# Kernel optimization log

Measured on AMD Instinct MI355X. Metric: run time of the kernel, lower is better.

Reference implementation:

```python
import jax, jax.numpy as jnp
import numpy as np

N = 25600            # 64 graphs x 400 ROIs
F_IN = 400
H = 128
E = 512000           # 8000 edges per graph
B = 64
G = 8
OUT = 2
NPG = 400            # nodes per graph
EPG = E // B         # edges per graph
BN_EPS = 1e-5


def _xavier(k, shape):
    lim = float(np.sqrt(6.0 / (shape[0] + shape[1])))
    return jax.random.uniform(k, shape, jnp.float32, -lim, lim)


def setup_inputs() -> dict:
    key = jax.random.key(0)
    ks = jax.random.split(key, 16)
    inp = {}
    inp["x"] = jax.random.normal(ks[0], (N, F_IN), jnp.float32)
    # within-graph random edges: local index + graph offset
    src_l = jax.random.randint(ks[1], (E,), 0, NPG, jnp.int32)
    dst_l = jax.random.randint(ks[2], (E,), 0, NPG, jnp.int32)
    off = (jnp.arange(E, dtype=jnp.int32) // EPG) * NPG
    inp["edge_index"] = jnp.stack([src_l + off, dst_l + off])
    inp["batch"] = (jnp.arange(N, dtype=jnp.int32) // NPG)
    inp["group_ids"] = jax.random.randint(ks[3], (N,), 0, G, jnp.int32)
    inp["ge"] = _xavier(ks[4], (G, 2))
    inp["he"] = _xavier(ks[5], (2, 2))
    dims = [(F_IN + 4, H), (H, H), (H, H)]
    for i, (di, do) in enumerate(dims):
        k1, k2 = jax.random.split(ks[6 + i])
        inp[f"w{i}a"] = _xavier(k1, (di, do))
        inp[f"b{i}a"] = jnp.zeros((do,), jnp.float32)
        inp[f"g{i}"] = jnp.ones((do,), jnp.float32)
        inp[f"be{i}"] = jnp.zeros((do,), jnp.float32)
        inp[f"w{i}b"] = _xavier(k2, (do, do))
        inp[f"b{i}b"] = jnp.zeros((do,), jnp.float32)
    inp["wfa"] = _xavier(ks[10], (H, H))
    inp["bfa"] = jnp.zeros((H,), jnp.float32)
    inp["wfb"] = _xavier(ks[11], (H, OUT))
    inp["bfb"] = jnp.zeros((OUT,), jnp.float32)
    return inp


def _bn(h, gamma, beta):
    # BatchNorm1d in training mode: stats over node dimension
    mu = jnp.mean(h, axis=0, keepdims=True)
    var = jnp.var(h, axis=0, keepdims=True)
    return gamma * (h - mu) * jax.lax.rsqrt(var + BN_EPS) + beta


def reference(x, edge_index, batch, group_ids, ge, he,
              w0a, b0a, g0, be0, w0b, b0b,
              w1a, b1a, g1, be1, w1b, b1b,
              w2a, b2a, g2, be2, w2b, b2b,
              wfa, bfa, wfb, bfb):
    n = x.shape[0]
    hemi = jnp.arange(n) % 2                      # [1::2] = 1
    h = jnp.concatenate([x, ge[group_ids], he[hemi]], axis=-1)  # [N, F_IN+4]
    src, dst = edge_index[0], edge_index[1]
    layers = [(w0a, b0a, g0, be0, w0b, b0b),
              (w1a, b1a, g1, be1, w1b, b1b),
              (w2a, b2a, g2, be2, w2b, b2b)]
    for wa, ba, g, be, wb, bb in layers:
        # GINConv (eps=0): x_i + sum_{(j,i)} x_j, then 2-layer MLP w/ batchnorm
        agg = jax.ops.segment_sum(h[src], dst, num_segments=N)
        z = h + agg
        z = jax.nn.relu(_bn(z @ wa + ba, g, be))  # dropout = identity (eval)
        h = jax.nn.relu(z @ wb + bb)              # outer ReLU from forward()
    pooled = jax.ops.segment_sum(h, batch, num_segments=B)  # global_add_pool
    return jax.nn.relu(pooled @ wfa + bfa) @ wfb + bfb
```

## Files before the change

### kernel.cpp

```cpp
#include <hip/hip_runtime.h>

#define N_NODES 25600
#define F_IN 400
#define NE 512000
#define NB 64
#define NPG 400
#define EPG 8000
#define BN_EPS 1e-5f
#define NBLK 256

typedef __attribute__((ext_vector_type(8))) short short8;
typedef __attribute__((ext_vector_type(4))) float floatx4;
typedef unsigned short us;
typedef unsigned long long u64;

__device__ __forceinline__ unsigned short f2bf(float f) {
    unsigned int u = __float_as_uint(f);
    u += 0x7FFF + ((u >> 16) & 1);
    return (unsigned short)(u >> 16);
}
__device__ __forceinline__ float bf2f(unsigned short s) {
    return __uint_as_float((unsigned int)s << 16);
}
__device__ __forceinline__ short u8bf(unsigned v) {
    return (short)(__float_as_uint((float)v) >> 16);
}
__device__ __forceinline__ void ast64(void* p, u64 v) {
    __hip_atomic_store((u64*)p, v, __ATOMIC_RELAXED, __HIP_MEMORY_SCOPE_AGENT);
}
__device__ __forceinline__ u64 pk4(unsigned short a, unsigned short b, unsigned short c, unsigned short d) {
    return (u64)a | ((u64)b << 16) | ((u64)c << 32) | ((u64)d << 48);
}

__device__ __forceinline__ void gsync_tree(unsigned* bar, int bid, int phase) {
    __syncthreads();
    if (threadIdx.x == 0) {
        unsigned* leaf = bar + 32 + (bid >> 4) * 32;
        unsigned v = __hip_atomic_fetch_add(leaf, 1u, __ATOMIC_RELAXED, __HIP_MEMORY_SCOPE_AGENT);
        if (v == (unsigned)(phase * 16 - 1))
            __hip_atomic_fetch_add(bar, 1u, __ATOMIC_RELAXED, __HIP_MEMORY_SCOPE_AGENT);
        while (__hip_atomic_load(bar, __ATOMIC_RELAXED, __HIP_MEMORY_SCOPE_AGENT) < (unsigned)(phase * 16))
            __builtin_amdgcn_s_sleep(8);
        asm volatile("" ::: "memory");
    }
    __syncthreads();
}

__device__ __forceinline__ void gbar4(unsigned* gc, int stage) {
    __syncthreads();
    if (threadIdx.x == 0) {
        __hip_atomic_fetch_add(gc, 1u, __ATOMIC_RELAXED, __HIP_MEMORY_SCOPE_AGENT);
        while (__hip_atomic_load(gc, __ATOMIC_RELAXED, __HIP_MEMORY_SCOPE_AGENT) < (unsigned)(stage * 4))
            __builtin_amdgcn_s_sleep(8);
        asm volatile("" ::: "memory");
    }
    __syncthreads();
}



__device__ __forceinline__ void ph_prep(unsigned char* sm, int g, int q, int bid, int tid,
        const int* __restrict__ src, const int* __restrict__ dst, us* __restrict__ SbBF,
        const float* __restrict__ wa0, const float* __restrict__ wa1, const float* __restrict__ wa2,
        const float* __restrict__ wb0, const float* __restrict__ wb1, const float* __restrict__ wb2,
        us* __restrict__ wt0, us* __restrict__ wtb0, us* __restrict__ wta1,
        us* __restrict__ wtb1, us* __restrict__ wta2, us* __restrict__ wtb2) {
    int r0 = q * 112;
    int* cnt = (int*)sm;
    for (int i = tid; i < 11200; i += 1024) cnt[i] = 0;
    __syncthreads();
    int ebase = g * EPG, nbase = g * NPG;
    for (int e = tid; e < EPG; e += 1024) {
        int d = dst[ebase + e] - nbase;
        int dr = d - r0;
        if ((unsigned)dr < 112u) {
            int s = src[ebase + e] - nbase;
            int idx = dr * NPG + s;
            atomicAdd(&cnt[idx >> 2], (int)(1u << ((idx & 3) * 8)));
        }
    }
    __syncthreads();
    const unsigned char* cb = (const unsigned char*)cnt;
    for (int i = tid; i < 112 * 112; i += 1024) {
        int rr = i / 112, c4 = (i % 112) * 4;
        int R = r0 + rr;
        ushort4 o;
#pragma unroll
        for (int j = 0; j < 4; ++j) {
            int c = c4 + j;
            unsigned v = (R < NPG && c < NPG) ? (unsigned)cb[rr * NPG + c] + (c == R ? 1u : 0u) : 0u;
            ((unsigned short*)&o)[j] = (unsigned short)u8bf(v);
        }
        *(ushort4*)&SbBF[((size_t)g * 448 + R) * 448 + c4] = o;
    }
    if (tid < 136) {
        int idx = bid * 136 + tid;
        if (idx < 14336) {
            int n = idx / 112, k0 = (idx % 112) * 4;
            unsigned short o[4];
#pragma unroll
            for (int j = 0; j < 4; ++j) {
                int k = k0 + j;
                o[j] = (k < 400) ? f2bf(wa0[(size_t)k * 128 + n]) : (unsigned short)0;
            }
            ast64(&wt0[(size_t)n * 448 + k0], pk4(o[0], o[1], o[2], o[3]));
        } else {
            int r2 = idx - 14336;
            int m = r2 >> 12, q2 = r2 & 4095;
            int n = q2 >> 5, k0 = (q2 & 31) * 4;
            const float* smat = (m == 0) ? wb0 : (m == 1) ? wa1 : (m == 2) ? wb1 : (m == 3) ? wa2 : wb2;
            us* dmat = (m == 0) ? wtb0 : (m == 1) ? wta1 : (m == 2) ? wtb1 : (m == 3) ? wta2 : wtb2;
            unsigned short o[4];
#pragma unroll
            for (int j = 0; j < 4; ++j) o[j] = f2bf(smat[(size_t)(k0 + j) * 128 + n]);
            ast64(&dmat[(size_t)n * 128 + k0], pk4(o[0], o[1], o[2], o[3]));
        }
    }
}


__device__ __forceinline__ void ph_embed(unsigned char* sm, int g, int q, int tid,
        const float* __restrict__ x, const us* __restrict__ wt0, const float* __restrict__ wa0,
        const int* __restrict__ gid, const float* __restrict__ ge, const float* __restrict__ he,
        us* __restrict__ tT0) {
    us (*Bf)[456] = (us(*)[456])sm;
    us (*As)[72] = (us(*)[72])(sm + 116736);
    float (*Wex)[128] = (float(*)[128])(sm + 135168);
    int nb = g * NPG + q * 100;
    int wave = tid >> 6, lane = tid & 63;
    int wrow = wave >> 2, wc4 = wave & 3;
    int fm = lane & 15, quad = lane >> 4;

    {
        short8 tp[7];
#pragma unroll
        for (int j = 0; j < 7; ++j) {
            int i = tid + j * 1024;
            int col = i / 56, kq = (i - col * 56) * 8;
            tp[j] = *(const short8*)(wt0 + (size_t)col * 448 + kq);
        }
#pragma unroll
        for (int j = 0; j < 7; ++j) {
            int i = tid + j * 1024;
            int col = i / 56, kq = (i - col * 56) * 8;
            *(short8*)&Bf[col][kq] = tp[j];
        }
    }
    for (int i = tid; i < 512; i += 1024)
        Wex[i >> 7][i & 127] = wa0[(size_t)(400 + (i >> 7)) * 128 + (i & 127)];

    floatx4 acc[2][2];
#pragma unroll
    for (int rt = 0; rt < 2; ++rt)
#pragma unroll
        for (int ct = 0; ct < 2; ++ct) acc[rt][ct] = (floatx4){0.f, 0.f, 0.f, 0.f};

    const int rA = tid >> 3, kcA = (tid & 7) * 8;
    float v[8];
    auto loadK = [&](int ks) {
        int kg = ks * 64 + kcA;
        if (rA < 100) {
            const float* ar = x + (size_t)(nb + rA) * F_IN;
            if (kg + 7 < 400) {
                float4 a = *(const float4*)(ar + kg);
                float4 b = *(const float4*)(ar + kg + 4);
                v[0] = a.x; v[1] = a.y; v[2] = a.z; v[3] = a.w;
                v[4] = b.x; v[5] = b.y; v[6] = b.z; v[7] = b.w;
            } else {
#pragma unroll
                for (int j = 0; j < 8; ++j) v[j] = (kg + j < 400) ? ar[kg + j] : 0.f;
            }
        } else {
#pragma unroll
            for (int j = 0; j < 8; ++j) v[j] = 0.f;
        }
    };

    loadK(0);
    for (int ks = 0; ks < 7; ++ks) {
        {
            short8 s;
#pragma unroll
            for (int j = 0; j < 8; ++j) s[j] = (short)f2bf(v[j]);
            *(short8*)&As[rA][kcA] = s;
        }
        __syncthreads();
        if (ks + 1 < 7) loadK(ks + 1);
#pragma unroll
        for (int k0l = 0; k0l < 64; k0l += 32) {
            short8 af[2], bf[2];
#pragma unroll
            for (int rt = 0; rt < 2; ++rt)
                af[rt] = *(const short8*)&As[wrow * 32 + rt * 16 + fm][k0l + quad * 8];
#pragma unroll
            for (int ct = 0; ct < 2; ++ct)
                bf[ct] = *(const short8*)&Bf[wc4 * 32 + ct * 16 + fm][ks * 64 + k0l + quad * 8];
#pragma unroll
            for (int rt = 0; rt < 2; ++rt)
#pragma unroll
                for (int ct = 0; ct < 2; ++ct)
                    acc[rt][ct] = __builtin_amdgcn_mfma_f32_16x16x32_bf16(
                        af[rt], bf[ct], acc[rt][ct], 0, 0, 0);
        }
        __syncthreads();
    }

#pragma unroll
    for (int rt = 0; rt < 2; ++rt)
#pragma unroll
        for (int ct = 0; ct < 2; ++ct) {
            int col = wc4 * 32 + ct * 16 + fm;
            int rl0 = wrow * 32 + rt * 16 + quad * 4;
            if (rl0 < 100) {
                unsigned short o[4];
#pragma unroll
                for (int r = 0; r < 4; ++r) {
                    int row = nb + rl0 + r;
                    int gv = gid[row];
                    float vv = acc[rt][ct][r]
                             + ge[gv * 2] * Wex[0][col] + ge[gv * 2 + 1] * Wex[1][col]
                             + he[(row & 1) * 2] * Wex[2][col] + he[(row & 1) * 2 + 1] * Wex[3][col];
                    o[r] = f2bf(vv);
                }
                ast64(&tT0[(size_t)col * N_NODES + nb + rl0], pk4(o[0], o[1], o[2], o[3]));
            }
        }
}


__device__ __forceinline__ void ph_agg(unsigned char* sm, int g, int q, int tid,
        const us* __restrict__ SbBF, const us* __restrict__ tTr, const float* __restrict__ ba,
        float* __restrict__ psum, float* __restrict__ psq, int bucket) {
    us (*Bf)[456] = (us(*)[456])sm;
    us (*zl)[136] = (us(*)[136])sm;
    float (*rs)[4][2][16] = (float(*)[4][2][16])(sm + 116736);
    float (*rq)[4][2][16] = (float(*)[4][2][16])(sm + 118784);
    int wave = tid >> 6, lane = tid & 63;
    int wrow = wave >> 2, wc4 = wave & 3;
    int fm = lane & 15, quad = lane >> 4;
    int node0 = g * NPG;

    {
        short8 tp[7];
        const short8 z8 = {0, 0, 0, 0, 0, 0, 0, 0};
#pragma unroll
        for (int j = 0; j < 7; ++j) {
            int i = tid + j * 1024;
            int col = i / 56, kq = (i - col * 56) * 8;
            tp[j] = (kq < 400) ? *(const short8*)(tTr + (size_t)col * N_NODES + node0 + kq) : z8;
        }
#pragma unroll
        for (int j = 0; j < 7; ++j) {
            int i = tid + j * 1024;
            int col = i / 56, kq = (i - col * 56) * 8;
            *(short8*)&Bf[col][kq] = tp[j];
        }
    }
    __syncthreads();

    floatx4 acc[2][2];
#pragma unroll
    for (int rt = 0; rt < 2; ++rt)
#pragma unroll
        for (int ct = 0; ct < 2; ++ct) acc[rt][ct] = (floatx4){0.f, 0.f, 0.f, 0.f};

    const us* abase = SbBF + ((size_t)g * 448 + q * 112) * 448;
#pragma unroll
    for (int ks = 0; ks < 7; ++ks) {
#pragma unroll
        for (int k0l = 0; k0l < 64; k0l += 32) {
            short8 af[2], bf[2];
#pragma unroll
            for (int rt = 0; rt < 2; ++rt)
                af[rt] = *(const short8*)(abase + (size_t)(wrow * 32 + rt * 16 + fm) * 448
                                          + ks * 64 + k0l + quad * 8);
#pragma unroll
            for (int ct = 0; ct < 2; ++ct)
                bf[ct] = *(const short8*)&Bf[wc4 * 32 + ct * 16 + fm][ks * 64 + k0l + quad * 8];
#pragma unroll
            for (int rt = 0; rt < 2; ++rt)
#pragma unroll
                for (int ct = 0; ct < 2; ++ct)
                    acc[rt][ct] = __builtin_amdgcn_mfma_f32_16x16x32_bf16(
                        af[rt], bf[ct], acc[rt][ct], 0, 0, 0);
        }
    }
    __syncthreads();

    int nrows = (q < 3) ? 112 : 64;
    float sc[2] = {0.f, 0.f}, sq2[2] = {0.f, 0.f};
#pragma unroll
    for (int rt = 0; rt < 2; ++rt)
#pragma unroll
        for (int ct = 0; ct < 2; ++ct) {
            int col = wc4 * 32 + ct * 16 + fm;
            int rl0 = wrow * 32 + rt * 16 + quad * 4;
            if (rl0 < nrows) {
                float bv = ba[col];
#pragma unroll
                for (int r = 0; r < 4; ++r) {
                    float vv = acc[rt][ct][r] + bv;
                    zl[rl0 + r][col] = f2bf(vv);
                    sc[ct] += vv;
                    sq2[ct] += vv * vv;
                }
            }
        }
#pragma unroll
    for (int ct = 0; ct < 2; ++ct) {
        sc[ct] += __shfl_xor(sc[ct], 16);
        sc[ct] += __shfl_xor(sc[ct], 32);
        sq2[ct] += __shfl_xor(sq2[ct], 16);
        sq2[ct] += __shfl_xor(sq2[ct], 32);
    }
    if (lane < 16) {
#pragma unroll
        for (int ct = 0; ct < 2; ++ct) { rs[wrow][wc4][ct][lane] = sc[ct]; rq[wrow][wc4][ct][lane] = sq2[ct]; }
    }
    __syncthreads();
    if (tid < 128) {
        int wc = tid >> 5, ct = (tid >> 4) & 1, f = tid & 15;
        float S = 0.f, Q = 0.f;
#pragma unroll
        for (int wr = 0; wr < 4; ++wr) { S += rs[wr][wc][ct][f]; Q += rq[wr][wc][ct][f]; }
        atomicAdd(&psum[bucket * 128 + tid], S);
        atomicAdd(&psq[bucket * 128 + tid], Q);
    }
}


template <int FINAL>
__device__ __forceinline__ void ph_post(unsigned char* sm, int g, int q, int tid,
        const float* __restrict__ psum, const float* __restrict__ psq,
        const float* __restrict__ gamma, const float* __restrict__ beta,
        const us* __restrict__ wtbP, const float* __restrict__ bb,
        const us* __restrict__ wanP, us* __restrict__ tTw, float& p0, float& p1) {
    us (*zl)[136] = (us(*)[136])sm;
    float* coefs = (float*)(sm + 34816);
    us (*Bw)[136] = (us(*)[136])(sm + 35840);
    int wave = tid >> 6, lane = tid & 63;
    int wrow = wave >> 2, wc4 = wave & 3;
    int fm = lane & 15, quad = lane >> 4;
    int nrows = (q < 3) ? 112 : 64;
    int nb = g * NPG + q * 112;

    short8 w1[2], w2[2];
#pragma unroll
    for (int j = 0; j < 2; ++j) {
        int i = tid + j * 1024;
        int col = i >> 4, kq = (i & 15) * 8;
        w1[j] = *(const short8*)(wtbP + (size_t)col * 128 + kq);
        if (!FINAL) w2[j] = *(const short8*)(wanP + (size_t)col * 128 + kq);
    }

    if (tid < 128) {
        float S = 0.f, Q = 0.f;
#pragma unroll
        for (int b = 0; b < 16; ++b) {
            S += __hip_atomic_load(&psum[b * 128 + tid], __ATOMIC_RELAXED, __HIP_MEMORY_SCOPE_AGENT);
            Q += __hip_atomic_load(&psq[b * 128 + tid], __ATOMIC_RELAXED, __HIP_MEMORY_SCOPE_AGENT);
        }
        float invn = 1.0f / (float)N_NODES;
        float mu = S * invn;
        float var = Q * invn - mu * mu;
        float a = gamma[tid] * rsqrtf(var + BN_EPS);
        coefs[tid] = a;
        coefs[128 + tid] = beta[tid] - a * mu;
    }
#pragma unroll
    for (int j = 0; j < 2; ++j) {
        int i = tid + j * 1024;
        int col = i >> 4, kq = (i & 15) * 8;
        *(short8*)&Bw[col][kq] = w1[j];
    }
    __syncthreads();
    for (int i = tid; i < 16384; i += 1024) {
        int rl = i >> 7, col = i & 127;
        float vv = bf2f(zl[rl][col]);
        zl[rl][col] = f2bf(fmaxf(coefs[col] * vv + coefs[128 + col], 0.f));
    }
    __syncthreads();

    floatx4 acc[2][2];
#pragma unroll
    for (int rt = 0; rt < 2; ++rt)
#pragma unroll
        for (int ct = 0; ct < 2; ++ct) acc[rt][ct] = (floatx4){0.f, 0.f, 0.f, 0.f};

#pragma unroll
    for (int ks = 0; ks < 2; ++ks)
#pragma unroll
        for (int k0l = 0; k0l < 64; k0l += 32) {
            short8 af[2], bf[2];
#pragma unroll
            for (int rt = 0; rt < 2; ++rt)
                af[rt] = *(const short8*)&zl[wrow * 32 + rt * 16 + fm][ks * 64 + k0l + quad * 8];
#pragma unroll
            for (int ct = 0; ct < 2; ++ct)
                bf[ct] = *(const short8*)&Bw[wc4 * 32 + ct * 16 + fm][ks * 64 + k0l + quad * 8];
#pragma unroll
            for (int rt = 0; rt < 2; ++rt)
#pragma unroll
                for (int ct = 0; ct < 2; ++ct)
                    acc[rt][ct] = __builtin_amdgcn_mfma_f32_16x16x32_bf16(
                        af[rt], bf[ct], acc[rt][ct], 0, 0, 0);
        }

    if (FINAL) {
#pragma unroll
        for (int rt = 0; rt < 2; ++rt)
#pragma unroll
            for (int ct = 0; ct < 2; ++ct) {
                int col = wc4 * 32 + ct * 16 + fm;
                int rl0 = wrow * 32 + rt * 16 + quad * 4;
                if (rl0 < nrows) {
                    float bv = bb[col];
                    float s = 0.f;
#pragma unroll
                    for (int r = 0; r < 4; ++r) s += fmaxf(acc[rt][ct][r] + bv, 0.f);
                    if (ct == 0) p0 += s; else p1 += s;
                }
            }
        return;
    }

    __syncthreads();
#pragma unroll
    for (int rt = 0; rt < 2; ++rt)
#pragma unroll
        for (int ct = 0; ct < 2; ++ct) {
            int col = wc4 * 32 + ct * 16 + fm;
            float bv = bb[col];
            int rl0 = wrow * 32 + rt * 16 + quad * 4;
#pragma unroll
            for (int r = 0; r < 4; ++r)
                zl[rl0 + r][col] = f2bf(fmaxf(acc[rt][ct][r] + bv, 0.f));
        }
#pragma unroll
    for (int j = 0; j < 2; ++j) {
        int i = tid + j * 1024;
        int col = i >> 4, kq = (i & 15) * 8;
        *(short8*)&Bw[col][kq] = w2[j];
    }
    __syncthreads();

#pragma unroll
    for (int rt = 0; rt < 2; ++rt)
#pragma unroll
        for (int ct = 0; ct < 2; ++ct) acc[rt][ct] = (floatx4){0.f, 0.f, 0.f, 0.f};

#pragma unroll
    for (int ks = 0; ks < 2; ++ks)
#pragma unroll
        for (int k0l = 0; k0l < 64; k0l += 32) {
            short8 af[2], bf[2];
#pragma unroll
            for (int rt = 0; rt < 2; ++rt)
                af[rt] = *(const short8*)&zl[wrow * 32 + rt * 16 + fm][ks * 64 + k0l + quad * 8];
#pragma unroll
            for (int ct = 0; ct < 2; ++ct)
                bf[ct] = *(const short8*)&Bw[wc4 * 32 + ct * 16 + fm][ks * 64 + k0l + quad * 8];
#pragma unroll
            for (int rt = 0; rt < 2; ++rt)
#pragma unroll
                for (int ct = 0; ct < 2; ++ct)
                    acc[rt][ct] = __builtin_amdgcn_mfma_f32_16x16x32_bf16(
                        af[rt], bf[ct], acc[rt][ct], 0, 0, 0);
        }

#pragma unroll
    for (int rt = 0; rt < 2; ++rt)
#pragma unroll
        for (int ct = 0; ct < 2; ++ct) {
            int col = wc4 * 32 + ct * 16 + fm;
            int rl0 = wrow * 32 + rt * 16 + quad * 4;
            if (rl0 < nrows) {
                unsigned short o[4];
#pragma unroll
                for (int r = 0; r < 4; ++r) o[r] = f2bf(acc[rt][ct][r]);
                ast64(&tTw[(size_t)col * N_NODES + nb + rl0], pk4(o[0], o[1], o[2], o[3]));
            }
        }
}


__global__ __launch_bounds__(1024, 4) void persist_all(
        const float* __restrict__ x, const int* __restrict__ esrc, const int* __restrict__ edst,
        const int* __restrict__ gid, const float* __restrict__ ge, const float* __restrict__ he,
        const float* __restrict__ wa0, const float* __restrict__ ba0, const float* __restrict__ gg0,
        const float* __restrict__ be0, const float* __restrict__ wb0, const float* __restrict__ bbias0,
        const float* __restrict__ wa1, const float* __restrict__ ba1, const float* __restrict__ gg1,
        const float* __restrict__ be1, const float* __restrict__ wb1, const float* __restrict__ bbias1,
        const float* __restrict__ wa2, const float* __restrict__ ba2, const float* __restrict__ gg2,
        const float* __restrict__ be2, const float* __restrict__ wb2, const float* __restrict__ bbias2,
        const float* __restrict__ wfa, const float* __restrict__ bfa,
        const float* __restrict__ wfb, const float* __restrict__ bfb,
        us* __restrict__ tT0, us* __restrict__ tT1, us* __restrict__ tT2,
        us* __restrict__ SbBF, float* __restrict__ pstat, unsigned* __restrict__ bar,
        us* __restrict__ wt0, us* __restrict__ wtb0, us* __restrict__ wta1,
        us* __restrict__ wtb1, us* __restrict__ wta2, us* __restrict__ wtb2,
        float* __restrict__ out) {
    __shared__ __align__(16) unsigned char sm[137216];
    int bid = blockIdx.x, tid = threadIdx.x;
    int g = (bid & 7) * 8 + ((bid >> 3) & 7);
    int q = bid >> 6;
    unsigned* gc = bar + 544 + g * 32;
    float* pooled = pstat + 12288;
    float p0 = 0.f, p1 = 0.f;

    ph_prep(sm, g, q, bid, tid, esrc, edst, SbBF, wa0, wa1, wa2, wb0, wb1, wb2,
            wt0, wtb0, wta1, wtb1, wta2, wtb2);
    gsync_tree(bar, bid, 1);

    ph_embed(sm, g, q, tid, x, wt0, wa0, gid, ge, he, tT0);
    gbar4(gc, 1);

    ph_agg(sm, g, q, tid, SbBF, tT0, ba0, pstat + 0, pstat + 2048, bid & 15);
    gsync_tree(bar, bid, 2);
    ph_post<0>(sm, g, q, tid, pstat + 0, pstat + 2048, gg0, be0, wtb0, bbias0, wta1, tT1, p0, p1);
    gbar4(gc, 2);

    ph_agg(sm, g, q, tid, SbBF, tT1, ba1, pstat + 4096, pstat + 6144, bid & 15);
    gsync_tree(bar, bid, 3);
    ph_post<0>(sm, g, q, tid, pstat + 4096, pstat + 6144, gg1, be1, wtb1, bbias1, wta2, tT2, p0, p1);
    gbar4(gc, 3);

    ph_agg(sm, g, q, tid, SbBF, tT2, ba2, pstat + 8192, pstat + 10240, bid & 15);
    gsync_tree(bar, bid, 4);
    ph_post<1>(sm, g, q, tid, pstat + 8192, pstat + 10240, gg2, be2, wtb2, bbias2, nullptr, nullptr, p0, p1);

    {
        int wave = tid >> 6, lane = tid & 63;
        int wrow = wave >> 2, wc4 = wave & 3;
        float (*red)[4][2][16] = (float(*)[4][2][16])sm;
        p0 += __shfl_xor(p0, 16); p0 += __shfl_xor(p0, 32);
        p1 += __shfl_xor(p1, 16); p1 += __shfl_xor(p1, 32);
        __syncthreads();
        if (lane < 16) { red[wrow][wc4][0][lane] = p0; red[wrow][wc4][1][lane] = p1; }
        __syncthreads();
        if (tid < 128) {
            int wc = tid >> 5, ct = (tid >> 4) & 1, f = tid & 15;
            float s = 0.f;
#pragma unroll
            for (int wr = 0; wr < 4; ++wr) s += red[wr][wc][ct][f];
            atomicAdd(&pooled[g * 128 + tid], s);
        }
    }
    gbar4(gc, 4);

    if (q == 0) {
        float* pl = (float*)sm;
        float* o0 = pl + 128;
        float* o1 = pl + 256;
        __syncthreads();
        if (tid < 128) {
            unsigned uv = __hip_atomic_load((const unsigned*)&pooled[g * 128 + tid],
                                            __ATOMIC_RELAXED, __HIP_MEMORY_SCOPE_AGENT);
            pl[tid] = __uint_as_float(uv);
        }
        __syncthreads();
        if (tid < 128) {
            float a = bfa[tid];
            for (int k = 0; k < 128; ++k) a += pl[k] * wfa[k * 128 + tid];
            float p2 = fmaxf(a, 0.f);
            o0[tid] = p2 * wfb[tid * 2 + 0];
            o1[tid] = p2 * wfb[tid * 2 + 1];
        }
        __syncthreads();
        if (tid == 0) {
            float a0 = bfb[0], a1 = bfb[1];
#pragma unroll
            for (int k = 0; k < 128; ++k) { a0 += o0[k]; a1 += o1[k]; }
            out[g * 2 + 0] = a0;
            out[g * 2 + 1] = a1;
        }
    }
}


extern "C" void kernel_launch(void* const* d_in, const int* in_sizes, int n_in,
                              void* d_out, int out_size, void* d_ws, size_t ws_size,
                              hipStream_t stream) {
    const float* x   = (const float*)d_in[0];
    const int* ei    = (const int*)d_in[1];
    const int* gid   = (const int*)d_in[3];
    const float* ge  = (const float*)d_in[4];
    const float* he  = (const float*)d_in[5];
    float* out = (float*)d_out;

    char* ws = (char*)d_ws;
    size_t o = 0;
    auto alloc = [&](size_t bytes) { char* p = ws + o; o += (bytes + 255) & ~(size_t)255; return p; };
    size_t tbytes = (size_t)128 * N_NODES * 2;
    us* tT0 = (us*)alloc(tbytes);
    us* tT1 = (us*)alloc(tbytes);
    us* tT2 = (us*)alloc(tbytes);
    us* SbBF = (us*)alloc((size_t)NB * 448 * 448 * 2);
    float* pstat = (float*)alloc(20480 * 4);
    unsigned* bar = (unsigned*)alloc(12288);
    us* wt0  = (us*)alloc(128 * 448 * 2);
    us* wtb0 = (us*)alloc(128 * 128 * 2);
    us* wta1 = (us*)alloc(128 * 128 * 2);
    us* wtb1 = (us*)alloc(128 * 128 * 2);
    us* wta2 = (us*)alloc(128 * 128 * 2);
    us* wtb2 = (us*)alloc(128 * 128 * 2);
    (void)ws_size; (void)in_sizes; (void)n_in; (void)out_size;

    hipMemsetAsync(pstat, 0, 81920 + 12288, stream);

    persist_all<<<NBLK, 1024, 0, stream>>>(
        x, ei, ei + NE, gid, ge, he,
        (const float*)d_in[6],  (const float*)d_in[7],  (const float*)d_in[8],
        (const float*)d_in[9],  (const float*)d_in[10], (const float*)d_in[11],
        (const float*)d_in[12], (const float*)d_in[13], (const float*)d_in[14],
        (const float*)d_in[15], (const float*)d_in[16], (const float*)d_in[17],
        (const float*)d_in[18], (const float*)d_in[19], (const float*)d_in[20],
        (const float*)d_in[21], (const float*)d_in[22], (const float*)d_in[23],
        (const float*)d_in[24], (const float*)d_in[25],
        (const float*)d_in[26], (const float*)d_in[27],
        tT0, tT1, tT2, SbBF, pstat, bar,
        wt0, wtb0, wta1, wtb1, wta2, wtb2,
        out);
}
```

Before: 248.1 us.

## Pack adjacency to 4-bit counts and keep block's slice resident in LDS

The per-graph dense adjacency (edge counts plus identity) is now stored as 4-bit nibbles instead of bf16. Each block loads its 112-row slice once into shared memory after the embed phase and reuses it for all three aggregation layers. This replaces repeated global reads of a large bf16 matrix with per-element nibble-to-bf16 unpacking in the MFMA loop and a larger LDS footprint. It risks wrong results if any multi-edge count plus self-loop reaches 16, and the larger LDS use may lower occupancy.

```diff
diff --git a/kernel.cpp b/kernel.cpp
--- a/kernel.cpp
+++ b/kernel.cpp
@@ -9,6 +9,9 @@
 #define BN_EPS 1e-5f
 #define NBLK 256
 
+#define A4OFF 129024
+#define SM_SIZE 158720
+
 typedef __attribute__((ext_vector_type(8))) short short8;
 typedef __attribute__((ext_vector_type(4))) float floatx4;
 typedef unsigned short us;
@@ -60,7 +63,7 @@
 
 
 __device__ __forceinline__ void ph_prep(unsigned char* sm, int g, int q, int bid, int tid,
-        const int* __restrict__ src, const int* __restrict__ dst, us* __restrict__ SbBF,
+        const int* __restrict__ src, const int* __restrict__ dst, unsigned char* __restrict__ Sb4,
         const float* __restrict__ wa0, const float* __restrict__ wa1, const float* __restrict__ wa2,
         const float* __restrict__ wb0, const float* __restrict__ wb1, const float* __restrict__ wb2,
         us* __restrict__ wt0, us* __restrict__ wtb0, us* __restrict__ wta1,
@@ -81,17 +84,17 @@
     }
     __syncthreads();
     const unsigned char* cb = (const unsigned char*)cnt;
-    for (int i = tid; i < 112 * 112; i += 1024) {
-        int rr = i / 112, c4 = (i % 112) * 4;
+    for (int i = tid; i < 112 * 56; i += 1024) {
+        int rr = i / 56, c8 = (i % 56) * 8;
         int R = r0 + rr;
-        ushort4 o;
-#pragma unroll
-        for (int j = 0; j < 4; ++j) {
-            int c = c4 + j;
+        unsigned pk = 0;
+#pragma unroll
+        for (int j = 0; j < 8; ++j) {
+            int c = c8 + j;
             unsigned v = (R < NPG && c < NPG) ? (unsigned)cb[rr * NPG + c] + (c == R ? 1u : 0u) : 0u;
-            ((unsigned short*)&o)[j] = (unsigned short)u8bf(v);
-        }
-        *(ushort4*)&SbBF[((size_t)g * 448 + R) * 448 + c4] = o;
+            pk |= (v & 15u) << (4 * j);
+        }
+        *(unsigned*)&Sb4[(size_t)g * 100352 + (size_t)R * 224 + (c8 >> 1)] = pk;
     }
     if (tid < 136) {
         int idx = bid * 136 + tid;
@@ -229,12 +232,13 @@
 
 
 __device__ __forceinline__ void ph_agg(unsigned char* sm, int g, int q, int tid,
-        const us* __restrict__ SbBF, const us* __restrict__ tTr, const float* __restrict__ ba,
+        const us* __restrict__ tTr, const float* __restrict__ ba,
         float* __restrict__ psum, float* __restrict__ psq, int bucket) {
     us (*Bf)[456] = (us(*)[456])sm;
     us (*zl)[136] = (us(*)[136])sm;
     float (*rs)[4][2][16] = (float(*)[4][2][16])(sm + 116736);
     float (*rq)[4][2][16] = (float(*)[4][2][16])(sm + 118784);
+    const unsigned char* A4 = sm + A4OFF;
     int wave = tid >> 6, lane = tid & 63;
     int wrow = wave >> 2, wc4 = wave & 3;
     int fm = lane & 15, quad = lane >> 4;
@@ -264,16 +268,20 @@
 #pragma unroll
         for (int ct = 0; ct < 2; ++ct) acc[rt][ct] = (floatx4){0.f, 0.f, 0.f, 0.f};
 
-    const us* abase = SbBF + ((size_t)g * 448 + q * 112) * 448;
 #pragma unroll
     for (int ks = 0; ks < 7; ++ks) {
 #pragma unroll
         for (int k0l = 0; k0l < 64; k0l += 32) {
             short8 af[2], bf[2];
 #pragma unroll
-            for (int rt = 0; rt < 2; ++rt)
-                af[rt] = *(const short8*)(abase + (size_t)(wrow * 32 + rt * 16 + fm) * 448
-                                          + ks * 64 + k0l + quad * 8);
+            for (int rt = 0; rt < 2; ++rt) {
+                int row = wrow * 32 + rt * 16 + fm;
+                unsigned aP = *(const unsigned*)(A4 + row * 232 + ks * 32 + (k0l >> 1) + quad * 4);
+                short8 s;
+#pragma unroll
+                for (int j = 0; j < 8; ++j) s[j] = u8bf((aP >> (4 * j)) & 15u);
+                af[rt] = s;
+            }
 #pragma unroll
             for (int ct = 0; ct < 2; ++ct)
                 bf[ct] = *(const short8*)&Bf[wc4 * 32 + ct * 16 + fm][ks * 64 + k0l + quad * 8];
@@ -496,11 +504,11 @@
         const float* __restrict__ wfa, const float* __restrict__ bfa,
         const float* __restrict__ wfb, const float* __restrict__ bfb,
         us* __restrict__ tT0, us* __restrict__ tT1, us* __restrict__ tT2,
-        us* __restrict__ SbBF, float* __restrict__ pstat, unsigned* __restrict__ bar,
+        unsigned char* __restrict__ Sb4, float* __restrict__ pstat, unsigned* __restrict__ bar,
         us* __restrict__ wt0, us* __restrict__ wtb0, us* __restrict__ wta1,
         us* __restrict__ wtb1, us* __restrict__ wta2, us* __restrict__ wtb2,
         float* __restrict__ out) {
-    __shared__ __align__(16) unsigned char sm[137216];
+    __shared__ __align__(16) unsigned char sm[SM_SIZE];
     int bid = blockIdx.x, tid = threadIdx.x;
     int g = (bid & 7) * 8 + ((bid >> 3) & 7);
     int q = bid >> 6;
@@ -508,24 +516,44 @@
     float* pooled = pstat + 12288;
     float p0 = 0.f, p1 = 0.f;
 
-    ph_prep(sm, g, q, bid, tid, esrc, edst, SbBF, wa0, wa1, wa2, wb0, wb1, wb2,
+    ph_prep(sm, g, q, bid, tid, esrc, edst, Sb4, wa0, wa1, wa2, wb0, wb1, wb2,
             wt0, wtb0, wta1, wtb1, wta2, wtb2);
     gsync_tree(bar, bid, 1);
 
     ph_embed(sm, g, q, tid, x, wt0, wa0, gid, ge, he, tT0);
+
+    u64 aP4[4];
+    {
+        const u64* gs = (const u64*)(Sb4 + (size_t)g * 100352 + (size_t)q * 25088);
+#pragma unroll
+        for (int j = 0; j < 4; ++j) {
+            int i = tid + j * 1024;
+            aP4[j] = (i < 3136) ? gs[i] : 0ull;
+        }
+    }
     gbar4(gc, 1);
-
-    ph_agg(sm, g, q, tid, SbBF, tT0, ba0, pstat + 0, pstat + 2048, bid & 15);
+    {
+#pragma unroll
+        for (int j = 0; j < 4; ++j) {
+            int i = tid + j * 1024;
+            if (i < 3584) {
+                int rr = i / 28, c = i - rr * 28;
+                *(u64*)(sm + A4OFF + rr * 232 + c * 8) = aP4[j];
+            }
+        }
+    }
+
+    ph_agg(sm, g, q, tid, tT0, ba0, pstat + 0, pstat + 2048, bid & 15);
     gsync_tree(bar, bid, 2);
     ph_post<0>(sm, g, q, tid, pstat + 0, pstat + 2048, gg0, be0, wtb0, bbias0, wta1, tT1, p0, p1);
     gbar4(gc, 2);
 
-    ph_agg(sm, g, q, tid, SbBF, tT1, ba1, pstat + 4096, pstat + 6144, bid & 15);
+    ph_agg(sm, g, q, tid, tT1, ba1, pstat + 4096, pstat + 6144, bid & 15);
     gsync_tree(bar, bid, 3);
     ph_post<0>(sm, g, q, tid, pstat + 4096, pstat + 6144, gg1, be1, wtb1, bbias1, wta2, tT2, p0, p1);
     gbar4(gc, 3);
 
-    ph_agg(sm, g, q, tid, SbBF, tT2, ba2, pstat + 8192, pstat + 10240, bid & 15);
+    ph_agg(sm, g, q, tid, tT2, ba2, pstat + 8192, pstat + 10240, bid & 15);
     gsync_tree(bar, bid, 4);
     ph_post<1>(sm, g, q, tid, pstat + 8192, pstat + 10240, gg2, be2, wtb2, bbias2, nullptr, nullptr, p0, p1);
 
@@ -595,7 +623,7 @@
     us* tT0 = (us*)alloc(tbytes);
     us* tT1 = (us*)alloc(tbytes);
     us* tT2 = (us*)alloc(tbytes);
-    us* SbBF = (us*)alloc((size_t)NB * 448 * 448 * 2);
+    unsigned char* Sb4 = (unsigned char*)alloc((size_t)NB * 100352);
     float* pstat = (float*)alloc(20480 * 4);
     unsigned* bar = (unsigned*)alloc(12288);
     us* wt0  = (us*)alloc(128 * 448 * 2);
@@ -618,7 +646,7 @@
         (const float*)d_in[21], (const float*)d_in[22], (const float*)d_in[23],
         (const float*)d_in[24], (const float*)d_in[25],
         (const float*)d_in[26], (const float*)d_in[27],
-        tT0, tT1, tT2, SbBF, pstat, bar,
+        tT0, tT1, tT2, Sb4, pstat, bar,
         wt0, wtb0, wta1, wtb1, wta2, wtb2,
         out);
 }
```

After: 218.9 us. 11.8% less time.

## Store dense adjacency as uint8 counts and use packed bf16 conversion instruction

Applied to the files above, without the earlier changes.

The per-graph dense adjacency-plus-identity matrix is now stored as 8-bit counts instead of bf16. The aggregation phase converts each count to bf16 in registers before the MFMA, which halves the global traffic for reading the adjacency in each of the three layers. Manual round-to-nearest bf16 conversions are replaced with the hardware v_cvt_pk_bf16_f32 packed instruction across the embed, BN-relu and output stores. A tile row that is always out of range is skipped with zeros. The costs are extra unpack ALU work per fragment, and counts are assumed to fit in 8 bits.

```diff
diff --git a/kernel.cpp b/kernel.cpp
--- a/kernel.cpp
+++ b/kernel.cpp
@@ -8,6 +8,7 @@
 #define EPG 8000
 #define BN_EPS 1e-5f
 #define NBLK 256
+#define SM_SIZE 137216
 
 typedef __attribute__((ext_vector_type(8))) short short8;
 typedef __attribute__((ext_vector_type(4))) float floatx4;
@@ -22,8 +23,10 @@
 __device__ __forceinline__ float bf2f(unsigned short s) {
     return __uint_as_float((unsigned int)s << 16);
 }
-__device__ __forceinline__ short u8bf(unsigned v) {
-    return (short)(__float_as_uint((float)v) >> 16);
+__device__ __forceinline__ unsigned cvtpk(float lo, float hi) {
+    unsigned r;
+    asm("v_cvt_pk_bf16_f32 %0, %1, %2" : "=v"(r) : "v"(lo), "v"(hi));
+    return r;
 }
 __device__ __forceinline__ void ast64(void* p, u64 v) {
     __hip_atomic_store((u64*)p, v, __ATOMIC_RELAXED, __HIP_MEMORY_SCOPE_AGENT);
@@ -60,7 +63,7 @@
 
 
 __device__ __forceinline__ void ph_prep(unsigned char* sm, int g, int q, int bid, int tid,
-        const int* __restrict__ src, const int* __restrict__ dst, us* __restrict__ SbBF,
+        const int* __restrict__ src, const int* __restrict__ dst, unsigned char* __restrict__ Sb8,
         const float* __restrict__ wa0, const float* __restrict__ wa1, const float* __restrict__ wa2,
         const float* __restrict__ wb0, const float* __restrict__ wb1, const float* __restrict__ wb2,
         us* __restrict__ wt0, us* __restrict__ wtb0, us* __restrict__ wta1,
@@ -81,17 +84,17 @@
     }
     __syncthreads();
     const unsigned char* cb = (const unsigned char*)cnt;
-    for (int i = tid; i < 112 * 112; i += 1024) {
-        int rr = i / 112, c4 = (i % 112) * 4;
+    for (int i = tid; i < 112 * 56; i += 1024) {
+        int rr = i / 56, c8 = (i % 56) * 8;
         int R = r0 + rr;
-        ushort4 o;
-#pragma unroll
-        for (int j = 0; j < 4; ++j) {
-            int c = c4 + j;
+        u64 pk = 0;
+#pragma unroll
+        for (int j = 0; j < 8; ++j) {
+            int c = c8 + j;
             unsigned v = (R < NPG && c < NPG) ? (unsigned)cb[rr * NPG + c] + (c == R ? 1u : 0u) : 0u;
-            ((unsigned short*)&o)[j] = (unsigned short)u8bf(v);
-        }
-        *(ushort4*)&SbBF[((size_t)g * 448 + R) * 448 + c4] = o;
+            pk |= (u64)(v & 255u) << (8 * j);
+        }
+        *(u64*)&Sb8[((size_t)g * 448 + R) * 448 + c8] = pk;
     }
     if (tid < 136) {
         int idx = bid * 136 + tid;
@@ -179,10 +182,12 @@
     loadK(0);
     for (int ks = 0; ks < 7; ++ks) {
         {
-            short8 s;
-#pragma unroll
-            for (int j = 0; j < 8; ++j) s[j] = (short)f2bf(v[j]);
-            *(short8*)&As[rA][kcA] = s;
+            union { unsigned w[4]; short8 s; } u;
+            u.w[0] = cvtpk(v[0], v[1]);
+            u.w[1] = cvtpk(v[2], v[3]);
+            u.w[2] = cvtpk(v[4], v[5]);
+            u.w[3] = cvtpk(v[6], v[7]);
+            *(short8*)&As[rA][kcA] = u.s;
         }
         __syncthreads();
         if (ks + 1 < 7) loadK(ks + 1);
@@ -212,24 +217,24 @@
             int col = wc4 * 32 + ct * 16 + fm;
             int rl0 = wrow * 32 + rt * 16 + quad * 4;
             if (rl0 < 100) {
-                unsigned short o[4];
+                float vv[4];
 #pragma unroll
                 for (int r = 0; r < 4; ++r) {
                     int row = nb + rl0 + r;
                     int gv = gid[row];
-                    float vv = acc[rt][ct][r]
-                             + ge[gv * 2] * Wex[0][col] + ge[gv * 2 + 1] * Wex[1][col]
-                             + he[(row & 1) * 2] * Wex[2][col] + he[(row & 1) * 2 + 1] * Wex[3][col];
-                    o[r] = f2bf(vv);
+                    vv[r] = acc[rt][ct][r]
+                          + ge[gv * 2] * Wex[0][col] + ge[gv * 2 + 1] * Wex[1][col]
+                          + he[(row & 1) * 2] * Wex[2][col] + he[(row & 1) * 2 + 1] * Wex[3][col];
                 }
-                ast64(&tT0[(size_t)col * N_NODES + nb + rl0], pk4(o[0], o[1], o[2], o[3]));
+                unsigned wlo = cvtpk(vv[0], vv[1]), whi = cvtpk(vv[2], vv[3]);
+                ast64(&tT0[(size_t)col * N_NODES + nb + rl0], (u64)wlo | ((u64)whi << 32));
             }
         }
 }
 
 
 __device__ __forceinline__ void ph_agg(unsigned char* sm, int g, int q, int tid,
-        const us* __restrict__ SbBF, const us* __restrict__ tTr, const float* __restrict__ ba,
+        const unsigned char* __restrict__ Sb8, const us* __restrict__ tTr, const float* __restrict__ ba,
         float* __restrict__ psum, float* __restrict__ psq, int bucket) {
     us (*Bf)[456] = (us(*)[456])sm;
     us (*zl)[136] = (us(*)[136])sm;
@@ -264,16 +269,32 @@
 #pragma unroll
         for (int ct = 0; ct < 2; ++ct) acc[rt][ct] = (floatx4){0.f, 0.f, 0.f, 0.f};
 
-    const us* abase = SbBF + ((size_t)g * 448 + q * 112) * 448;
+    const unsigned char* a8 = Sb8 + ((size_t)g * 448 + q * 112) * 448;
 #pragma unroll
     for (int ks = 0; ks < 7; ++ks) {
 #pragma unroll
         for (int k0l = 0; k0l < 64; k0l += 32) {
             short8 af[2], bf[2];
 #pragma unroll
-            for (int rt = 0; rt < 2; ++rt)
-                af[rt] = *(const short8*)(abase + (size_t)(wrow * 32 + rt * 16 + fm) * 448
-                                          + ks * 64 + k0l + quad * 8);
+            for (int rt = 0; rt < 2; ++rt) {
+                if (wrow == 3 && rt == 1) {
+                    af[rt] = (short8){0, 0, 0, 0, 0, 0, 0, 0};
+                } else {
+                    u64 v8 = *(const u64*)(a8 + (size_t)(wrow * 32 + rt * 16 + fm) * 448
+                                           + ks * 64 + k0l + quad * 8);
+                    unsigned lo = (unsigned)v8, hi = (unsigned)(v8 >> 32);
+                    float f0 = (float)(lo & 255u), f1 = (float)((lo >> 8) & 255u);
+                    float f2 = (float)((lo >> 16) & 255u), f3 = (float)(lo >> 24);
+                    float f4 = (float)(hi & 255u), f5 = (float)((hi >> 8) & 255u);
+                    float f6 = (float)((hi >> 16) & 255u), f7 = (float)(hi >> 24);
+                    union { unsigned w[4]; short8 s; } u;
+                    u.w[0] = __builtin_amdgcn_perm(__float_as_uint(f1), __float_as_uint(f0), 0x07060302u);
+                    u.w[1] = __builtin_amdgcn_perm(__float_as_uint(f3), __float_as_uint(f2), 0x07060302u);
+                    u.w[2] = __builtin_amdgcn_perm(__float_as_uint(f5), __float_as_uint(f4), 0x07060302u);
+                    u.w[3] = __builtin_amdgcn_perm(__float_as_uint(f7), __float_as_uint(f6), 0x07060302u);
+                    af[rt] = u.s;
+                }
+            }
 #pragma unroll
             for (int ct = 0; ct < 2; ++ct)
                 bf[ct] = *(const short8*)&Bf[wc4 * 32 + ct * 16 + fm][ks * 64 + k0l + quad * 8];
@@ -374,10 +395,14 @@
         *(short8*)&Bw[col][kq] = w1[j];
     }
     __syncthreads();
-    for (int i = tid; i < 16384; i += 1024) {
-        int rl = i >> 7, col = i & 127;
-        float vv = bf2f(zl[rl][col]);
-        zl[rl][col] = f2bf(fmaxf(coefs[col] * vv + coefs[128 + col], 0.f));
+    for (int i = tid; i < 8192; i += 1024) {
+        int rl = i >> 6, c2 = i & 63;
+        unsigned* zw = (unsigned*)&zl[rl][0];
+        unsigned w = zw[c2];
+        int col = c2 * 2;
+        float lo = fmaxf(coefs[col] * bf2f((us)(w & 0xffff)) + coefs[128 + col], 0.f);
+        float hi = fmaxf(coefs[col + 1] * bf2f((us)(w >> 16)) + coefs[129 + col], 0.f);
+        zw[c2] = cvtpk(lo, hi);
     }
     __syncthreads();
 
@@ -475,10 +500,9 @@
             int col = wc4 * 32 + ct * 16 + fm;
             int rl0 = wrow * 32 + rt * 16 + quad * 4;
             if (rl0 < nrows) {
-                unsigned short o[4];
-#pragma unroll
-                for (int r = 0; r < 4; ++r) o[r] = f2bf(acc[rt][ct][r]);
-                ast64(&tTw[(size_t)col * N_NODES + nb + rl0], pk4(o[0], o[1], o[2], o[3]));
+                unsigned wlo = cvtpk(acc[rt][ct][0], acc[rt][ct][1]);
+                unsigned whi = cvtpk(acc[rt][ct][2], acc[rt][ct][3]);
+                ast64(&tTw[(size_t)col * N_NODES + nb + rl0], (u64)wlo | ((u64)whi << 32));
             }
         }
 }
@@ -496,11 +520,11 @@
         const float* __restrict__ wfa, const float* __restrict__ bfa,
         const float* __restrict__ wfb, const float* __restrict__ bfb,
         us* __restrict__ tT0, us* __restrict__ tT1, us* __restrict__ tT2,
-        us* __restrict__ SbBF, float* __restrict__ pstat, unsigned* __restrict__ bar,
+        unsigned char* __restrict__ Sb8, float* __restrict__ pstat, unsigned* __restrict__ bar,
         us* __restrict__ wt0, us* __restrict__ wtb0, us* __restrict__ wta1,
         us* __restrict__ wtb1, us* __restrict__ wta2, us* __restrict__ wtb2,
         float* __restrict__ out) {
-    __shared__ __align__(16) unsigned char sm[137216];
+    __shared__ __align__(16) unsigned char sm[SM_SIZE];
     int bid = blockIdx.x, tid = threadIdx.x;
     int g = (bid & 7) * 8 + ((bid >> 3) & 7);
     int q = bid >> 6;
@@ -508,24 +532,24 @@
     float* pooled = pstat + 12288;
     float p0 = 0.f, p1 = 0.f;
 
-    ph_prep(sm, g, q, bid, tid, esrc, edst, SbBF, wa0, wa1, wa2, wb0, wb1, wb2,
+    ph_prep(sm, g, q, bid, tid, esrc, edst, Sb8, wa0, wa1, wa2, wb0, wb1, wb2,
             wt0, wtb0, wta1, wtb1, wta2, wtb2);
     gsync_tree(bar, bid, 1);
 
     ph_embed(sm, g, q, tid, x, wt0, wa0, gid, ge, he, tT0);
     gbar4(gc, 1);
 
-    ph_agg(sm, g, q, tid, SbBF, tT0, ba0, pstat + 0, pstat + 2048, bid & 15);
+    ph_agg(sm, g, q, tid, Sb8, tT0, ba0, pstat + 0, pstat + 2048, bid & 15);
     gsync_tree(bar, bid, 2);
     ph_post<0>(sm, g, q, tid, pstat + 0, pstat + 2048, gg0, be0, wtb0, bbias0, wta1, tT1, p0, p1);
     gbar4(gc, 2);
 
-    ph_agg(sm, g, q, tid, SbBF, tT1, ba1, pstat + 4096, pstat + 6144, bid & 15);
+    ph_agg(sm, g, q, tid, Sb8, tT1, ba1, pstat + 4096, pstat + 6144, bid & 15);
     gsync_tree(bar, bid, 3);
     ph_post<0>(sm, g, q, tid, pstat + 4096, pstat + 6144, gg1, be1, wtb1, bbias1, wta2, tT2, p0, p1);
     gbar4(gc, 3);
 
-    ph_agg(sm, g, q, tid, SbBF, tT2, ba2, pstat + 8192, pstat + 10240, bid & 15);
+    ph_agg(sm, g, q, tid, Sb8, tT2, ba2, pstat + 8192, pstat + 10240, bid & 15);
     gsync_tree(bar, bid, 4);
     ph_post<1>(sm, g, q, tid, pstat + 8192, pstat + 10240, gg2, be2, wtb2, bbias2, nullptr, nullptr, p0, p1);
 
@@ -595,7 +619,7 @@
     us* tT0 = (us*)alloc(tbytes);
     us* tT1 = (us*)alloc(tbytes);
     us* tT2 = (us*)alloc(tbytes);
-    us* SbBF = (us*)alloc((size_t)NB * 448 * 448 * 2);
+    unsigned char* Sb8 = (unsigned char*)alloc((size_t)NB * 448 * 448);
     float* pstat = (float*)alloc(20480 * 4);
     unsigned* bar = (unsigned*)alloc(12288);
     us* wt0  = (us*)alloc(128 * 448 * 2);
@@ -618,7 +642,7 @@
         (const float*)d_in[21], (const float*)d_in[22], (const float*)d_in[23],
         (const float*)d_in[24], (const float*)d_in[25],
         (const float*)d_in[26], (const float*)d_in[27],
-        tT0, tT1, tT2, SbBF, pstat, bar,
+        tT0, tT1, tT2, Sb8, pstat, bar,
         wt0, wtb0, wta1, wtb1, wta2, wtb2,
         out);
 }
```

After: 230.0 us. 1.08x faster.
